# Optimization experiments

Hardware: AMD Instinct MI355X
Metric: run time of the kernel (lower is better)

## Reference

```python
import jax, jax.numpy as jnp
import numpy as np

B, NS, NQ = 128, 128, 512
D_IN, D_OUT = 256, 64


def setup_inputs() -> dict:
    key = jax.random.key(0)
    ks = jax.random.split(key, 6)
    return {
        "phi_support": jax.random.normal(ks[0], (B, NS, D_IN), dtype=jnp.float32),
        "y_support": jax.random.normal(ks[1], (B, NS, D_OUT), dtype=jnp.float32),
        "phi_query": jax.random.normal(ks[2], (B, NQ, D_IN), dtype=jnp.float32),
        "y_query": jax.random.normal(ks[3], (B, NQ, D_OUT), dtype=jnp.float32),
        # xavier-uniform-ish params
        "m_prior": jax.random.uniform(ks[4], (D_IN, D_OUT), minval=-1.0, maxval=1.0) * np.sqrt(6.0 / (D_IN + D_OUT)),
        "S_inv_prior_asym": jax.random.uniform(ks[5], (D_IN, D_IN), minval=-1.0, maxval=1.0) * np.sqrt(6.0 / (2 * D_IN)),
        "sig_eps": jnp.array([0.1], dtype=jnp.float32),
    }


def reference(phi_support, y_support, phi_query, y_query, m_prior, S_inv_prior_asym, sig_eps):
    alpha = 1.0
    d_out = m_prior.shape[1]
    # prior precision (symmetric PSD by construction) and natural-param prior mean
    S_inv_prior = alpha * (S_inv_prior_asym @ S_inv_prior_asym.T)          # [D_in, D_in]
    m_prior_nat = S_inv_prior @ m_prior                                     # [D_in, D_out]
    # posterior precision / covariance per task (nobs > 0 branch)
    S_inv = jnp.einsum('bni,bnj->bij', phi_support, phi_support) + S_inv_prior  # [B, D_in, D_in]
    S = jnp.linalg.inv(S_inv)                                               # batched small inverse
    rhs = jnp.einsum('bni,bnk->bik', phi_support, y_support) + m_prior_nat  # [B, D_in, D_out]
    m = S @ rhs                                                             # [B, D_in, D_out]
    # predictive mean and spread
    mu = phi_query @ m                                                      # [B, Q, D_out]
    spread_fac = 1.0 + jnp.einsum('bqi,bij,bqj->bq', phi_query, S, phi_query)  # [B, Q]
    # sig = spread_fac (x) (eye * sig_eps) : diagonal [B, Q, D_out, D_out]
    diag = jnp.eye(d_out, dtype=mu.dtype) * sig_eps                         # [D_out, D_out]
    sig = spread_fac[..., None, None] * diag
    # nll: logdet of diagonal sig + quadratic form with its inverse (diag -> reciprocal)
    logdet = d_out * (jnp.log(spread_fac) + jnp.log(sig_eps))               # [B, Q]
    resid = y_query - mu
    quadf = jnp.sum(resid * resid, axis=-1) / (spread_fac * sig_eps)        # [B, Q]
    nll = logdet.mean() + quadf.mean()
    return mu, sig, nll
```

## Files before the change

### kernel.cpp

```cpp
#include <hip/hip_runtime.h>
#include <math.h>

#define B_T   128
#define NS    128
#define NQ    512
#define DIN   256
#define DOUT  64

#define MU_SIZE  (B_T*NQ*DOUT)
#define SIG_SIZE (B_T*NQ*DOUT*DOUT)
#define NLL_IDX  (MU_SIZE + SIG_SIZE)

typedef double v4df __attribute__((ext_vector_type(4)));

__device__ __forceinline__ void dmap(int fl, int kq, int mrow, int rr,
                                     int& lr, int& lc) {
    if (fl == 0)      { lr = kq * 4 + rr; lc = mrow; }
    else if (fl == 1) { lr = kq + 4 * rr; lc = mrow; }
    else if (fl == 2) { lr = mrow; lc = kq * 4 + rr; }
    else              { lr = mrow; lc = kq + 4 * rr; }
}

__global__ void k_mfma_probe(double* __restrict__ FLAGD) {
    int l = threadIdx.x;
// ... 139 lines not shown
            for (int s = 0; s < 4; ++s) {
                int j = j0 + 4 * tx + s;
                Gb[i * 256 + j] = acc[r][s] + Sp[i * 256 + j];
            }
        }
    }
}

__global__ __launch_bounds__(256) void k_build_rhs(const float* __restrict__ PHI,
                                                   const float* __restrict__ Y,
                                                   const double* __restrict__ MPN,
                                                   double* __restrict__ RHS,
                                                   const double* __restrict__ FLAGD) {
    __shared__ float As[128][64];
    __shared__ float Ys[128][64];
    int b = blockIdx.x, i0 = blockIdx.y * 64, tid = threadIdx.x;
    const float* Pb = PHI + b * (NS * DIN);
    const float* Yb = Y + b * (NS * DOUT);
    for (int idx = tid; idx < 128 * 64; idx += 256) {
        int n = idx >> 6, c = idx & 63;
        As[n][c] = Pb[n * 256 + i0 + c];
        Ys[n][c] = Yb[n * 64 + c];
    }
    __syncthreads();
    double* Rb = RHS + b * 16384;
    int fl = (int)FLAGD[0];
    if (fl < 4) {
        int lane = tid & 63, w = tid >> 6;
        int mrow = lane & 15, kq = lane >> 4;
        v4df acc[4];
#pragma unroll
        for (int t = 0; t < 4; ++t) acc[t] = (v4df){0.0, 0.0, 0.0, 0.0};
        for (int ks = 0; ks < 128; ks += 4) {
            double a = (double)As[ks + kq][w * 16 + mrow];
#pragma unroll
            for (int t = 0; t < 4; ++t) {
                double bb = (double)Ys[ks + kq][t * 16 + mrow];
                acc[t] = __builtin_amdgcn_mfma_f64_16x16x4f64(a, bb, acc[t], 0, 0, 0);
            }
        }
#pragma unroll
        for (int t = 0; t < 4; ++t) {
#pragma unroll
            for (int rr = 0; rr < 4; ++rr) {
                int lr, lc; dmap(fl, kq, mrow, rr, lr, lc);
                int i = i0 + w * 16 + lr;
                int kc = t * 16 + lc;
                Rb[i * 64 + kc] = acc[t][rr] + MPN[i * 64 + kc];
            }
        }
    } else {
        int tx = tid & 15, ty = tid >> 4;
        double acc[4][4];
#pragma unroll
        for (int r = 0; r < 4; ++r)
#pragma unroll
            for (int s = 0; s < 4; ++s) acc[r][s] = 0.0;
        for (int n = 0; n < 128; ++n) {
            float a0 = As[n][4 * ty + 0], a1 = As[n][4 * ty + 1];
            float a2 = As[n][4 * ty + 2], a3 = As[n][4 * ty + 3];
            float y0 = Ys[n][4 * tx + 0], y1 = Ys[n][4 * tx + 1];
            float y2 = Ys[n][4 * tx + 2], y3 = Ys[n][4 * tx + 3];
            acc[0][0] += (double)a0 * y0; acc[0][1] += (double)a0 * y1;
            acc[0][2] += (double)a0 * y2; acc[0][3] += (double)a0 * y3;
            acc[1][0] += (double)a1 * y0; acc[1][1] += (double)a1 * y1;
            acc[1][2] += (double)a1 * y2; acc[1][3] += (double)a1 * y3;
            acc[2][0] += (double)a2 * y0; acc[2][1] += (double)a2 * y1;
            acc[2][2] += (double)a2 * y2; acc[2][3] += (double)a2 * y3;
            acc[3][0] += (double)a3 * y0; acc[3][1] += (double)a3 * y1;
            acc[3][2] += (double)a3 * y2; acc[3][3] += (double)a3 * y3;
        }
#pragma unroll
        for (int r = 0; r < 4; ++r) {
            int i = i0 + 4 * ty + r;
#pragma unroll
            for (int s = 0; s < 4; ++s) {
                int kc = 4 * tx + s;
                Rb[i * 64 + kc] = acc[r][s] + MPN[i * 64 + kc];
            }
        }
    }
}

__global__ __launch_bounds__(256) void k_potrf64(const double* __restrict__ G,
                                                 double* __restrict__ LT,
                                                 double* __restrict__ LI,
                                                 int kb) {
    __shared__ double D[64][65];
    __shared__ double T[64][33];
    __shared__ double C[32][33];
    __shared__ double L11s[16 * 17];
    __shared__ double DINVs[16];
    int b = blockIdx.x, tid = threadIdx.x;
    int o = kb * 64;
    const double* Gb = G + b * 65536;
    double* LTb = LT + b * 65536;
    double* LIb = LI + b * 16384 + kb * 4096;
    for (int idx = tid; idx < 4096; idx += 256) {
        int r = idx >> 6, c = idx & 63;
        D[r][c] = Gb[(o + r) * 256 + o + c];
    }
    __syncthreads();
    for (int p0 = 0; p0 < 64; p0 += 16) {
        if (tid < 64) {
            int lane = tid;
            double a[16];
            if (lane < 16) {
#pragma unroll
                for (int p = 0; p < 16; ++p) a[p] = D[p0 + lane][p0 + p];
            }
#pragma unroll
            for (int p = 0; p < 16; ++p) {
                double dp = __shfl(a[p], p);
                double d = sqrt(fmax(dp, 1e-300));
                double inv = 1.0 / d;
                if (lane == p) { a[p] = d; DINVs[p] = inv; }
                else if (lane > p) a[p] *= inv;
#pragma unroll
                for (int p2 = p + 1; p2 < 16; ++p2) {
                    double cc = __shfl(a[p], p2);
                    if (lane > p) a[p2] -= a[p] * cc;
                }
            }
            if (lane < 16) {
#pragma unroll
                for (int p = 0; p < 16; ++p) {
                    if (p <= lane) {
                        L11s[lane * 17 + p] = a[p];
                        D[p0 + lane][p0 + p] = a[p];
                    }
                }
            }
        }
        __syncthreads();
        int nsolve = 48 - p0;
        if (tid < nsolve) {
            int rr = p0 + 16 + tid;
            double x[16];
#pragma unroll
            for (int p = 0; p < 16; ++p) {
                double s = D[rr][p0 + p];
#pragma unroll
                for (int p2 = 0; p2 < 16; ++p2) {
                    if (p2 < p) s -= L11s[p * 17 + p2] * x[p2];
                }
                x[p] = s * DINVs[p];
                D[rr][p0 + p] = x[p];
            }
        }
        __syncthreads();
        int rem = nsolve;
        for (int idx = tid; idx < rem * rem; idx += 256) {
            int i2 = idx / rem, j2 = idx - i2 * rem;
            if (j2 <= i2) {
                int i = p0 + 16 + i2, j = p0 + 16 + j2;
                double s = 0.0;
#pragma unroll
                for (int p = 0; p < 16; ++p) s += D[i][p0 + p] * D[j][p0 + p];
                D[i][j] -= s;
            }
        }
        __syncthreads();
    }
    for (int idx = tid; idx < 4096; idx += 256) {
        int c = idx >> 6, r = idx & 63;
        if (r >= c) LTb[(o + c) * 256 + (o + r)] = D[r][c];
    }
    if (tid < 64) {
        int g = tid >> 5, j = tid & 31;
        int off = g * 32;
        double x[32];
#pragma unroll
        for (int i = 0; i < 32; ++i) {
            double s = (i == j) ? 1.0 : 0.0;
#pragma unroll
            for (int k = 0; k < i; ++k) {
                double lv = D[off + i][off + k];
                s -= (k >= j) ? lv * x[k] : 0.0;
            }
            double inv = 1.0 / D[off + i][off + i];
            x[i] = (i >= j) ? s * inv : 0.0;
        }
#pragma unroll
        for (int i = 0; i < 32; ++i) T[off + i][j] = x[i];
    }
    __syncthreads();
    for (int idx = tid; idx < 1024; idx += 256) {
        int r = idx >> 5, c = idx & 31;
        double s = 0.0;
#pragma unroll
        for (int p = 0; p < 32; ++p) s += D[32 + r][p] * T[p][c];
        C[r][c] = s;
    }
    __syncthreads();
    for (int idx = tid; idx < 1024; idx += 256) {
        int r = idx >> 5, c = idx & 31;
        double s = 0.0;
#pragma unroll
        for (int p = 0; p < 32; ++p) s += T[32 + r][p] * C[p][c];
        D[32 + r][c] = -s;
    }
    __syncthreads();
    for (int idx = tid; idx < 4096; idx += 256) {
        int p = idx >> 6, c = idx & 63;
        double v;
        if (c < 32) v = (p < 32) ? T[c][p] : 0.0;
        else        v = (p < 32) ? D[c][p] : T[c][p - 32];
        LIb[p * 64 + c] = v;
    }
}

__global__ __launch_bounds__(256) void k_trsm64(const double* __restrict__ G,
                                                const double* __restrict__ LI,
                                                double* __restrict__ LT,
                                                int kb,
                                                const double* __restrict__ FLAGD) {
    __shared__ double Gs[64][65];
    __shared__ double Ls[64][65];
    int b = blockIdx.x;
    int i0 = (kb + 1 + blockIdx.y) * 64;
    int o = kb * 64;
    int tid = threadIdx.x;
    const double* Gb = G + b * 65536;
    const double* LIb = LI + b * 16384 + kb * 4096;
    double* LTb = LT + b * 65536;
    for (int idx = tid; idx < 4096; idx += 256) {
        int r = idx >> 6, c = idx & 63;
        Gs[r][c] = Gb[(i0 + r) * 256 + o + c];
        Ls[r][c] = LIb[idx];
    }
    __syncthreads();
    int fl = (int)FLAGD[0];
    if (fl < 4) {
        int lane = tid & 63, w = tid >> 6;
        int mrow = lane & 15, kq = lane >> 4;
        v4df acc[4];
#pragma unroll
        for (int t = 0; t < 4; ++t) acc[t] = (v4df){0.0, 0.0, 0.0, 0.0};
        for (int ks = 0; ks < 64; ks += 4) {
            double a = Gs[w * 16 + mrow][ks + kq];
#pragma unroll
            for (int t = 0; t < 4; ++t) {
                double bb = Ls[ks + kq][t * 16 + mrow];
                acc[t] = __builtin_amdgcn_mfma_f64_16x16x4f64(a, bb, acc[t], 0, 0, 0);
            }
        }
#pragma unroll
        for (int t = 0; t < 4; ++t) {
#pragma unroll
            for (int rr = 0; rr < 4; ++rr) {
                int lr, lc; dmap(fl, kq, mrow, rr, lr, lc);
                int r = w * 16 + lr;
                int c = t * 16 + lc;
                LTb[(o + c) * 256 + i0 + r] = acc[t][rr];
            }
        }
    } else {
        int tx = tid & 15, ty = tid >> 4;
        double acc[4][4];
#pragma unroll
        for (int r = 0; r < 4; ++r)
#pragma unroll
            for (int s = 0; s < 4; ++s) acc[r][s] = 0.0;
        for (int kk = 0; kk < 64; ++kk) {
            double a0 = Gs[4 * ty + 0][kk], a1 = Gs[4 * ty + 1][kk];
            double a2 = Gs[4 * ty + 2][kk], a3 = Gs[4 * ty + 3][kk];
            double b0 = Ls[kk][4 * tx + 0], b1 = Ls[kk][4 * tx + 1];
            double b2 = Ls[kk][4 * tx + 2], b3 = Ls[kk][4 * tx + 3];
            acc[0][0] += a0 * b0; acc[0][1] += a0 * b1; acc[0][2] += a0 * b2; acc[0][3] += a0 * b3;
            acc[1][0] += a1 * b0; acc[1][1] += a1 * b1; acc[1][2] += a1 * b2; acc[1][3] += a1 * b3;
            acc[2][0] += a2 * b0; acc[2][1] += a2 * b1; acc[2][2] += a2 * b2; acc[2][3] += a2 * b3;
            acc[3][0] += a3 * b0; acc[3][1] += a3 * b1; acc[3][2] += a3 * b2; acc[3][3] += a3 * b3;
        }
#pragma unroll
        for (int r = 0; r < 4; ++r)
#pragma unroll
            for (int s = 0; s < 4; ++s)
                LTb[(o + 4 * tx + s) * 256 + i0 + 4 * ty + r] = acc[r][s];
    }
}

__global__ __launch_bounds__(256) void k_syrk64(const double* __restrict__ LT,
                                                double* __restrict__ G,
                                                int kb,
                                                const double* __restrict__ FLAGD) {
    __shared__ double LiT[64][65];
    __shared__ double LjT[64][65];
    int b = blockIdx.x, py = blockIdx.y;
    int ti = 0;
    while (((ti + 1) * (ti + 2)) / 2 <= py) ti++;
    int tj = py - (ti * (ti + 1)) / 2;
    int i0 = (kb + 1 + ti) * 64, j0 = (kb + 1 + tj) * 64;
    int o = kb * 64;
    int tid = threadIdx.x;
    const double* LTb = LT + b * 65536;
    double* Gb = G + b * 65536;
    for (int idx = tid; idx < 4096; idx += 256) {
        int p = idx >> 6, r = idx & 63;
        LiT[p][r] = LTb[(o + p) * 256 + i0 + r];
        LjT[p][r] = LTb[(o + p) * 256 + j0 + r];
    }
    __syncthreads();
    int fl = (int)FLAGD[0];
    if (fl < 4) {
        int lane = tid & 63, w = tid >> 6;
        int mrow = lane & 15, kq = lane >> 4;
        v4df acc[4];
#pragma unroll
        for (int t = 0; t < 4; ++t) acc[t] = (v4df){0.0, 0.0, 0.0, 0.0};
        for (int ks = 0; ks < 64; ks += 4) {
            double a = LiT[ks + kq][w * 16 + mrow];
#pragma unroll
            for (int t = 0; t < 4; ++t) {
                double bb = LjT[ks + kq][t * 16 + mrow];
                acc[t] = __builtin_amdgcn_mfma_f64_16x16x4f64(a, bb, acc[t], 0, 0, 0);
            }
        }
#pragma unroll
        for (int t = 0; t < 4; ++t) {
#pragma unroll
            for (int rr = 0; rr < 4; ++rr) {
                int lr, lc; dmap(fl, kq, mrow, rr, lr, lc);
                int gi = i0 + w * 16 + lr;
                int gj = j0 + t * 16 + lc;
                Gb[gi * 256 + gj] -= acc[t][rr];
            }
        }
    } else {
        int tx = tid & 15, ty = tid >> 4;
        double acc[4][4];
#pragma unroll
        for (int r = 0; r < 4; ++r)
#pragma unroll
            for (int s = 0; s < 4; ++s) acc[r][s] = 0.0;
        for (int kk = 0; kk < 64; ++kk) {
            double a0 = LiT[kk][4 * ty + 0], a1 = LiT[kk][4 * ty + 1];
            double a2 = LiT[kk][4 * ty + 2], a3 = LiT[kk][4 * ty + 3];
            double b0 = LjT[kk][4 * tx + 0], b1 = LjT[kk][4 * tx + 1];
            double b2 = LjT[kk][4 * tx + 2], b3 = LjT[kk][4 * tx + 3];
            acc[0][0] += a0 * b0; acc[0][1] += a0 * b1; acc[0][2] += a0 * b2; acc[0][3] += a0 * b3;
            acc[1][0] += a1 * b0; acc[1][1] += a1 * b1; acc[1][2] += a1 * b2; acc[1][3] += a1 * b3;
            acc[2][0] += a2 * b0; acc[2][1] += a2 * b1; acc[2][2] += a2 * b2; acc[2][3] += a2 * b3;
            acc[3][0] += a3 * b0; acc[3][1] += a3 * b1; acc[3][2] += a3 * b2; acc[3][3] += a3 * b3;
        }
#pragma unroll
        for (int r = 0; r < 4; ++r) {
            int gi = i0 + 4 * ty + r;
#pragma unroll
            for (int s = 0; s < 4; ++s) {
                int gj = j0 + 4 * tx + s;
                Gb[gi * 256 + gj] -= acc[r][s];
            }
        }
    }
}

__global__ __launch_bounds__(256) void k_diaginv(const double* __restrict__ LT,
                                                 double* __restrict__ TI,
                                                 float* __restrict__ TIF) {
    __shared__ double SHD[8192];
    int b = blockIdx.x, tid = threadIdx.x;
    const double* LTb = LT + b * 65536;
    double* TIb = TI + b * 65536;
    float* TIFb = TIF + b * 65536;
    for (int idx = tid; idx < 65536; idx += 256) {
        int i = idx >> 8, k = idx & 255;
        if (k > i) { TIb[idx] = 0.0; TIFb[idx] = 0.0f; }
    }
    for (int idx = tid; idx < 8192; idx += 256) {
        int g = idx >> 10, rem = idx & 1023, k = rem >> 5, i = rem & 31;
        SHD[idx] = LTb[(32 * g + k) * 256 + 32 * g + i];
    }
    __syncthreads();
    int g = tid >> 5, j = tid & 31;
    const double* D = SHD + g * 1024;
    double x[32];
#pragma unroll
    for (int i = 0; i < 32; ++i) {
        double s = (i == j) ? 1.0 : 0.0;
#pragma unroll
        for (int k = 0; k < i; ++k) {
            double lv = D[k * 32 + i];
            s -= (k >= j) ? lv * x[k] : 0.0;
        }
        double inv = 1.0 / D[i * 32 + i];
        x[i] = (i >= j) ? s * inv : 0.0;
    }
#pragma unroll
    for (int i = 0; i < 32; ++i) {
        int gi = 32 * g + i, gj = 32 * g + j;
        TIb[gi * 256 + gj] = x[i];
        TIFb[gi * 256 + gj] = (float)x[i];
    }
}

__global__ __launch_bounds__(256) void k_trinv(const double* __restrict__ LT,
                                               double* __restrict__ TI,
                                               float* __restrict__ TIF) {
    __shared__ double XS[8][1024];
    int b = blockIdx.x, J = blockIdx.y;
    int tid = threadIdx.x, j = tid & 31, ig = tid >> 5;
    const double* LTb = LT + b * 65536;
    double* TIb = TI + b * 65536;
    float* TIFb = TIF + b * 65536;
    double* Bsh = XS[7];

    for (int idx = tid; idx < 1024; idx += 256) {
        int kk = idx >> 5, c = idx & 31;
        XS[J][idx] = TIb[(32 * J + kk) * 256 + 32 * J + c];
    }
    __syncthreads();

    for (int I = J + 1; I < 8; ++I) {
        double acc[4] = {0.0, 0.0, 0.0, 0.0};
        for (int K = J; K < I; ++K) {
            for (int idx = tid; idx < 1024; idx += 256) {
                int kk = idx >> 5, i2 = idx & 31;
                Bsh[idx] = LTb[(32 * K + kk) * 256 + 32 * I + i2];
            }
            __syncthreads();
            const double* Xk = XS[K];
            for (int kk = 0; kk < 32; ++kk) {
                double tv = Xk[kk * 32 + j];
#pragma unroll
                for (int r = 0; r < 4; ++r)
                    acc[r] += Bsh[kk * 32 + ig * 4 + r] * tv;
            }
            __syncthreads();
        }
#pragma unroll
        for (int r = 0; r < 4; ++r) Bsh[(ig * 4 + r) * 32 + j] = acc[r];
        __syncthreads();
        double c[4] = {0.0, 0.0, 0.0, 0.0};
        for (int k = 0; k < 32; ++k) {
            double bv = Bsh[k * 32 + j];
#pragma unroll
            for (int r = 0; r < 4; ++r)
                c[r] -= TIb[(32 * I + ig * 4 + r) * 256 + 32 * I + k] * bv;
        }
#pragma unroll
        for (int r = 0; r < 4; ++r) {
            int gi = 32 * I + ig * 4 + r, gj = 32 * J + j;
            TIb[gi * 256 + gj] = c[r];
            TIFb[gi * 256 + gj] = (float)c[r];
            if (I < 7) XS[I][(ig * 4 + r) * 32 + j] = c[r];
        }
        __syncthreads();
    }
}

__global__ __launch_bounds__(256) void k_gemm_Z(const double* __restrict__ TI,
                                                const double* __restrict__ RHS,
                                                double* __restrict__ Z,
                                                const double* __restrict__ FLAGD) {
    __shared__ double As[64][65];
    __shared__ double Bs[64][65];
    int b = blockIdx.x, i0 = blockIdx.y * 64;
    int tid = threadIdx.x;
    const double* TIb = TI + b * 65536;
    const double* Rb = RHS + b * 16384;
    double* Zb = Z + b * 16384;
    int fl = (int)FLAGD[0];
    if (fl < 4) {
        int lane = tid & 63, w = tid >> 6;
        int mrow = lane & 15, kq = lane >> 4;
        v4df acc[4];
#pragma unroll
        for (int t = 0; t < 4; ++t) acc[t] = (v4df){0.0, 0.0, 0.0, 0.0};
        for (int k0 = 0; k0 <= i0; k0 += 64) {
            for (int idx = tid; idx < 4096; idx += 256) {
                int r = idx >> 6, kk = idx & 63;
                As[r][kk] = TIb[(i0 + r) * 256 + k0 + kk];
                Bs[r][kk] = Rb[(k0 + r) * 64 + kk];
            }
            __syncthreads();
            for (int ks = 0; ks < 64; ks += 4) {
                double a = As[w * 16 + mrow][ks + kq];
#pragma unroll
                for (int t = 0; t < 4; ++t) {
                    double bb = Bs[ks + kq][t * 16 + mrow];
                    acc[t] = __builtin_amdgcn_mfma_f64_16x16x4f64(a, bb, acc[t], 0, 0, 0);
                }
            }
            __syncthreads();
        }
#pragma unroll
        for (int t = 0; t < 4; ++t) {
#pragma unroll
            for (int rr = 0; rr < 4; ++rr) {
                int lr, lc; dmap(fl, kq, mrow, rr, lr, lc);
                Zb[(i0 + w * 16 + lr) * 64 + t * 16 + lc] = acc[t][rr];
            }
        }
    } else {
        int c = tid & 63, rg = tid >> 6;
        double acc[16];
#pragma unroll
        for (int r = 0; r < 16; ++r) acc[r] = 0.0;
        for (int k0 = 0; k0 <= i0; k0 += 64) {
            for (int idx = tid; idx < 4096; idx += 256) {
                int r = idx >> 6, kk = idx & 63;
                As[r][kk] = TIb[(i0 + r) * 256 + k0 + kk];
                Bs[r][kk] = Rb[(k0 + r) * 64 + kk];
            }
            __syncthreads();
            for (int kk = 0; kk < 64; ++kk) {
                double bv = Bs[kk][c];
#pragma unroll
                for (int r = 0; r < 16; ++r)
                    acc[r] += As[rg * 16 + r][kk] * bv;
            }
            __syncthreads();
        }
#pragma unroll
        for (int r = 0; r < 16; ++r)
            Zb[(i0 + rg * 16 + r) * 64 + c] = acc[r];
    }
}

__global__ __launch_bounds__(256) void k_gemm_M(const double* __restrict__ TI,
                                                const double* __restrict__ Z,
                                                double* __restrict__ M,
                                                const double* __restrict__ FLAGD) {
    __shared__ double As[64][65];
    __shared__ double Bs[64][65];
    int b = blockIdx.x, i0 = blockIdx.y * 64;
    int tid = threadIdx.x;
    const double* TIb = TI + b * 65536;
// ... 151 lines not shown
        float dx = y.x - v.x, dy = y.y - v.y, dz = y.z - v.z, dw = y.w - v.w;
        float qs = dx * dx + dy * dy + dz * dz + dw * dw;
        qs += __shfl_down(qs, 8, 16);
        qs += __shfl_down(qs, 4, 16);
        qs += __shfl_down(qs, 2, 16);
        qs += __shfl_down(qs, 1, 16);
        if (tx == 0) {
            float sp = 1.0f + PSUM[(size_t)(b * 4 + 0) * 512 + q]
                            + PSUM[(size_t)(b * 4 + 1) * 512 + q]
                            + PSUM[(size_t)(b * 4 + 2) * 512 + q]
                            + PSUM[(size_t)(b * 4 + 3) * 512 + q];
            SPREAD[b * 512 + q] = sp;
            float val = 64.0f * (logf(sp) + logf(se)) + qs / (sp * se);
            nred[ty * 4 + r] = (double)val;
        }
    }
    __syncthreads();
    for (int s = 32; s > 0; s >>= 1) {
        if (tid < s) nred[tid] += nred[tid + s];
        __syncthreads();
    }
    if (tid == 0) atomicAdd(NLLACC, nred[0] * (1.0 / 65536.0));
}

__global__ void k_nll_final(const double* __restrict__ NLLACC,
                            float* __restrict__ out) {
    if (threadIdx.x == 0) out[NLL_IDX] = (float)NLLACC[0];
}

__global__ __launch_bounds__(256) void k_sig(const float* __restrict__ SPREAD,
                                             const float* __restrict__ SE,
                                             float* __restrict__ out) {
    __shared__ float sv_s;
    int bq = blockIdx.x, tid = threadIdx.x;
    if (tid == 0) sv_s = SPREAD[bq] * SE[0];
    __syncthreads();
    float sv = sv_s;
    float* base = out + (size_t)MU_SIZE + (size_t)bq * 4096;
    int i = tid >> 2;
    int jb = (tid & 3) << 4;
    int d = i - jb;
    float vals[16];
#pragma unroll
    for (int t = 0; t < 16; ++t) vals[t] = (t == d) ? sv : 0.0f;
    float4* p = (float4*)(base + tid * 16);
    p[0] = make_float4(vals[0], vals[1], vals[2], vals[3]);
    p[1] = make_float4(vals[4], vals[5], vals[6], vals[7]);
    p[2] = make_float4(vals[8], vals[9], vals[10], vals[11]);
    p[3] = make_float4(vals[12], vals[13], vals[14], vals[15]);
}

extern "C" void kernel_launch(void* const* d_in, const int* in_sizes, int n_in,
                              void* d_out, int out_size, void* d_ws, size_t ws_size,
                              hipStream_t stream) {
    const float* PHI_S = (const float*)d_in[0];
    const float* Y_S   = (const float*)d_in[1];
    const float* PHI_Q = (const float*)d_in[2];
    const float* Y_Q   = (const float*)d_in[3];
    const float* MP    = (const float*)d_in[4];
    const float* AP    = (const float*)d_in[5];
    const float* SE    = (const float*)d_in[6];
    float* out = (float*)d_out;

    double* scratch = (double*)(out + MU_SIZE);
    double* G    = scratch;
    double* LT   = G + 8388608;
    double* RHS  = LT + 8388608;
    double* Z    = RHS + 2097152;
    double* TI   = Z + 2097152;
    double* Spd  = TI + 8388608;
    double* MPN  = Spd + 65536;
    double* LI   = MPN + 16384;
    float*  TIF  = (float*)(LI + 2097152);
    float*  PSUM = TIF + 8388608;
    float*  SPREAD = (float*)d_ws;
    double* NLLACC = (double*)((char*)d_ws + 65536 * 4);
    double* FLAGD  = (double*)((char*)d_ws + 65536 * 4 + 8);

    k_mfma_probe <<<1, 64, 0, stream>>>(FLAGD);
    k_prior_sp   <<<256, 256, 0, stream>>>(AP, Spd, NLLACC);
    k_prior_mpn  <<<256, 64, 0, stream>>>(Spd, MP, MPN);
    k_build_G    <<<dim3(B_T, 10), 256, 0, stream>>>(PHI_S, Spd, G, FLAGD);
    k_build_rhs  <<<dim3(B_T, 4), 256, 0, stream>>>(PHI_S, Y_S, MPN, RHS, FLAGD);
    const int syrk_pairs[3] = {6, 3, 1};
    for (int kb = 0; kb < 4; ++kb) {
        k_potrf64<<<B_T, 256, 0, stream>>>(G, LT, LI, kb);
        if (kb < 3) {
            k_trsm64<<<dim3(B_T, 3 - kb), 256, 0, stream>>>(G, LI, LT, kb, FLAGD);
            k_syrk64<<<dim3(B_T, syrk_pairs[kb]), 256, 0, stream>>>(LT, G, kb, FLAGD);
        }
    }
    k_diaginv    <<<B_T, 256, 0, stream>>>(LT, TI, TIF);
    k_trinv      <<<dim3(B_T, 7), 256, 0, stream>>>(LT, TI, TIF);
    k_gemm_Z     <<<dim3(B_T, 4), 256, 0, stream>>>(TI, RHS, Z, FLAGD);
    k_gemm_M     <<<dim3(B_T, 4), 256, 0, stream>>>(TI, Z, RHS, FLAGD);
    k_spread_gemm<<<dim3(B_T, 8, 4), 256, 0, stream>>>(PHI_Q, TIF, PSUM);
    k_mu_nll     <<<dim3(B_T, 8), 256, 0, stream>>>(PHI_Q, RHS, Y_Q, PSUM, SE,
                                                    SPREAD, NLLACC, out);
    k_nll_final  <<<1, 64, 0, stream>>>(NLLACC, out);
    k_sig        <<<65536, 256, 0, stream>>>(SPREAD, SE, out);
}
```

Baseline: 2.074 ms.

## Fuse blocked Cholesky into one per-batch kernel and use 64-wide triangular inverse

Replaces the per-panel potrf/trsm/syrk launch sequence (about ten launches) with a single kernel per batch. That kernel loops over the four 64-column panels and does the factor, the panel solve and the trailing update in place. The triangular inverse moves from 32-wide blocks to 64-wide blocks, reusing the per-panel diagonal inverses LI from the Cholesky step. The aim is to cut launch overhead and redundant diagonal inversion. In exchange, it serialises all work within one block per batch (only 128 blocks), drops the MFMA f64 path in favour of scalar FMA loops, and loses cross-block parallelism in trsm/syrk.

```diff
diff --git a/kernel.cpp b/kernel.cpp
--- a/kernel.cpp
+++ b/kernel.cpp
@@ -245,368 +245,321 @@
     }
 }
 
-__global__ __launch_bounds__(256) void k_potrf64(const double* __restrict__ G,
-                                                 double* __restrict__ LT,
-                                                 double* __restrict__ LI,
-                                                 int kb) {
-    __shared__ double D[64][65];
-    __shared__ double T[64][33];
-    __shared__ double C[32][33];
-    __shared__ double L11s[16 * 17];
-    __shared__ double DINVs[16];
+__global__ __launch_bounds__(256) void k_cholf(double* __restrict__ G,
+                                               double* __restrict__ LT,
+                                               double* __restrict__ LI) {
+    __shared__ double S[8192];
+#define DD(r, c)  S[(r) * 65 + (c)]
+#define TT(i, j)  S[4160 + (i) * 33 + (j)]
+#define CC(r, c)  S[6272 + (r) * 33 + (c)]
+    double* LL = S + 7328;
+    double* DV = S + 7600;
+    double* S1 = S;
+    double* S2 = S + 4096;
     int b = blockIdx.x, tid = threadIdx.x;
-    int o = kb * 64;
-    const double* Gb = G + b * 65536;
+    double* Gb = G + b * 65536;
     double* LTb = LT + b * 65536;
-    double* LIb = LI + b * 16384 + kb * 4096;
-    for (int idx = tid; idx < 4096; idx += 256) {
-        int r = idx >> 6, c = idx & 63;
-        D[r][c] = Gb[(o + r) * 256 + o + c];
-    }
-    __syncthreads();
-    for (int p0 = 0; p0 < 64; p0 += 16) {
+    double* LIbase = LI + b * 16384;
+
+    for (int kb = 0; kb < 4; ++kb) {
+        int o = kb * 64;
+        double* LIb = LIbase + kb * 4096;
+        for (int idx = tid; idx < 4096; idx += 256) {
+            int r = idx >> 6, c = idx & 63;
+            DD(r, c) = Gb[(o + r) * 256 + o + c];
+        }
+        __syncthreads();
+        for (int p0 = 0; p0 < 64; p0 += 16) {
+            if (tid < 64) {
+                int lane = tid;
+                double a[16];
+                if (lane < 16) {
+#pragma unroll
+                    for (int p = 0; p < 16; ++p) a[p] = DD(p0 + lane, p0 + p);
+                }
+#pragma unroll
+                for (int p = 0; p < 16; ++p) {
+                    double dp = __shfl(a[p], p);
+                    double d = sqrt(fmax(dp, 1e-300));
+                    double inv = 1.0 / d;
+                    if (lane == p) { a[p] = d; DV[p] = inv; }
+                    else if (lane > p) a[p] *= inv;
+#pragma unroll
+                    for (int p2 = p + 1; p2 < 16; ++p2) {
+                        double cc = __shfl(a[p], p2);
+                        if (lane > p) a[p2] -= a[p] * cc;
+                    }
+                }
+                if (lane < 16) {
+#pragma unroll
+                    for (int p = 0; p < 16; ++p) {
+                        if (p <= lane) {
+                            LL[lane * 17 + p] = a[p];
+                            DD(p0 + lane, p0 + p) = a[p];
+                        }
+                    }
+                }
+            }
+            __syncthreads();
+            int nsolve = 48 - p0;
+            if (tid < nsolve) {
+                int rr = p0 + 16 + tid;
+                double x[16];
+#pragma unroll
+                for (int p = 0; p < 16; ++p) {
+                    double s = DD(rr, p0 + p);
+#pragma unroll
+                    for (int p2 = 0; p2 < 16; ++p2) {
+                        if (p2 < p) s -= LL[p * 17 + p2] * x[p2];
+                    }
+                    x[p] = s * DV[p];
+                    DD(rr, p0 + p) = x[p];
+                }
+            }
+            __syncthreads();
+            int rem = nsolve;
+            for (int idx = tid; idx < rem * rem; idx += 256) {
+                int i2 = idx / rem, j2 = idx - i2 * rem;
+                if (j2 <= i2) {
+                    int i = p0 + 16 + i2, j = p0 + 16 + j2;
+                    double s = 0.0;
+#pragma unroll
+                    for (int p = 0; p < 16; ++p) s += DD(i, p0 + p) * DD(j, p0 + p);
+                    DD(i, j) -= s;
+                }
+            }
+            __syncthreads();
+        }
+        for (int idx = tid; idx < 4096; idx += 256) {
+            int c = idx >> 6, r = idx & 63;
+            if (r >= c) LTb[(o + c) * 256 + (o + r)] = DD(r, c);
+        }
         if (tid < 64) {
-            int lane = tid;
-            double a[16];
-            if (lane < 16) {
-#pragma unroll
-                for (int p = 0; p < 16; ++p) a[p] = D[p0 + lane][p0 + p];
-            }
-#pragma unroll
-            for (int p = 0; p < 16; ++p) {
-                double dp = __shfl(a[p], p);
-                double d = sqrt(fmax(dp, 1e-300));
-                double inv = 1.0 / d;
-                if (lane == p) { a[p] = d; DINVs[p] = inv; }
-                else if (lane > p) a[p] *= inv;
-#pragma unroll
-                for (int p2 = p + 1; p2 < 16; ++p2) {
-                    double cc = __shfl(a[p], p2);
-                    if (lane > p) a[p2] -= a[p] * cc;
-                }
-            }
-            if (lane < 16) {
-#pragma unroll
-                for (int p = 0; p < 16; ++p) {
-                    if (p <= lane) {
-                        L11s[lane * 17 + p] = a[p];
-                        D[p0 + lane][p0 + p] = a[p];
+            int g = tid >> 5, j = tid & 31;
+            int off = g * 32;
+            double x[32];
+#pragma unroll
+            for (int i = 0; i < 32; ++i) {
+                double s = (i == j) ? 1.0 : 0.0;
+#pragma unroll
+                for (int k = 0; k < i; ++k) {
+                    double lv = DD(off + i, off + k);
+                    s -= (k >= j) ? lv * x[k] : 0.0;
+                }
+                double inv = 1.0 / DD(off + i, off + i);
+                x[i] = (i >= j) ? s * inv : 0.0;
+            }
+#pragma unroll
+            for (int i = 0; i < 32; ++i) TT(off + i, j) = x[i];
+        }
+        __syncthreads();
+        for (int idx = tid; idx < 1024; idx += 256) {
+            int r = idx >> 5, c = idx & 31;
+            double s = 0.0;
+#pragma unroll
+            for (int p = 0; p < 32; ++p) s += DD(32 + r, p) * TT(p, c);
+            CC(r, c) = s;
+        }
+        __syncthreads();
+        for (int idx = tid; idx < 1024; idx += 256) {
+            int r = idx >> 5, c = idx & 31;
+            double s = 0.0;
+#pragma unroll
+            for (int p = 0; p < 32; ++p) s += TT(32 + r, p) * CC(p, c);
+            DD(32 + r, c) = -s;
+        }
+        __syncthreads();
+        double v[16];
+#pragma unroll
+        for (int u = 0; u < 16; ++u) {
+            int idx = tid + u * 256;
+            int p = idx >> 6, c = idx & 63;
+            v[u] = (c < 32) ? ((p < 32) ? TT(c, p) : 0.0)
+                            : ((p < 32) ? DD(c, p) : TT(c, p - 32));
+        }
+        __syncthreads();
+#pragma unroll
+        for (int u = 0; u < 16; ++u) S1[tid + u * 256] = v[u];
+        __syncthreads();
+        for (int idx = tid; idx < 4096; idx += 256) LIb[idx] = S1[idx];
+        for (int rb = kb + 1; rb < 4; ++rb) {
+            int i0 = rb * 64;
+            for (int idx = tid; idx < 4096; idx += 256) {
+                int r = idx >> 6, kk = idx & 63;
+                S2[kk * 64 + r] = Gb[(i0 + r) * 256 + o + kk];
+            }
+            __syncthreads();
+            int tx = tid & 15, ty = tid >> 4;
+            double acc[4][4];
+#pragma unroll
+            for (int r = 0; r < 4; ++r)
+#pragma unroll
+                for (int s = 0; s < 4; ++s) acc[r][s] = 0.0;
+            for (int kk = 0; kk < 64; ++kk) {
+                double a0 = S2[kk * 64 + 4 * ty + 0], a1 = S2[kk * 64 + 4 * ty + 1];
+                double a2 = S2[kk * 64 + 4 * ty + 2], a3 = S2[kk * 64 + 4 * ty + 3];
+                double b0 = S1[kk * 64 + 4 * tx + 0], b1 = S1[kk * 64 + 4 * tx + 1];
+                double b2 = S1[kk * 64 + 4 * tx + 2], b3 = S1[kk * 64 + 4 * tx + 3];
+                acc[0][0] += a0 * b0; acc[0][1] += a0 * b1; acc[0][2] += a0 * b2; acc[0][3] += a0 * b3;
+                acc[1][0] += a1 * b0; acc[1][1] += a1 * b1; acc[1][2] += a1 * b2; acc[1][3] += a1 * b3;
+                acc[2][0] += a2 * b0; acc[2][1] += a2 * b1; acc[2][2] += a2 * b2; acc[2][3] += a2 * b3;
+                acc[3][0] += a3 * b0; acc[3][1] += a3 * b1; acc[3][2] += a3 * b2; acc[3][3] += a3 * b3;
+            }
+#pragma unroll
+            for (int r = 0; r < 4; ++r)
+#pragma unroll
+                for (int s = 0; s < 4; ++s)
+                    LTb[(o + 4 * tx + s) * 256 + i0 + 4 * ty + r] = acc[r][s];
+            __syncthreads();
+        }
+        for (int ti2 = kb + 1; ti2 < 4; ++ti2) {
+            for (int tj2 = kb + 1; tj2 <= ti2; ++tj2) {
+                int i0 = ti2 * 64, j0 = tj2 * 64;
+                for (int idx = tid; idx < 4096; idx += 256) {
+                    int p = idx >> 6, r = idx & 63;
+                    S1[idx] = LTb[(o + p) * 256 + i0 + r];
+                    S2[idx] = LTb[(o + p) * 256 + j0 + r];
+                }
+                __syncthreads();
+                int tx = tid & 15, ty = tid >> 4;
+                double acc[4][4];
+#pragma unroll
+                for (int r = 0; r < 4; ++r)
+#pragma unroll
+                    for (int s = 0; s < 4; ++s) acc[r][s] = 0.0;
+                for (int kk = 0; kk < 64; ++kk) {
+                    double a0 = S1[kk * 64 + 4 * ty + 0], a1 = S1[kk * 64 + 4 * ty + 1];
+                    double a2 = S1[kk * 64 + 4 * ty + 2], a3 = S1[kk * 64 + 4 * ty + 3];
+                    double b0 = S2[kk * 64 + 4 * tx + 0], b1 = S2[kk * 64 + 4 * tx + 1];
+                    double b2 = S2[kk * 64 + 4 * tx + 2], b3 = S2[kk * 64 + 4 * tx + 3];
+                    acc[0][0] += a0 * b0; acc[0][1] += a0 * b1; acc[0][2] += a0 * b2; acc[0][3] += a0 * b3;
+                    acc[1][0] += a1 * b0; acc[1][1] += a1 * b1; acc[1][2] += a1 * b2; acc[1][3] += a1 * b3;
+                    acc[2][0] += a2 * b0; acc[2][1] += a2 * b1; acc[2][2] += a2 * b2; acc[2][3] += a2 * b3;
+                    acc[3][0] += a3 * b0; acc[3][1] += a3 * b1; acc[3][2] += a3 * b2; acc[3][3] += a3 * b3;
+                }
+#pragma unroll
+                for (int r = 0; r < 4; ++r) {
+                    int gi = i0 + 4 * ty + r;
+#pragma unroll
+                    for (int s = 0; s < 4; ++s) {
+                        int gj = j0 + 4 * tx + s;
+                        Gb[gi * 256 + gj] -= acc[r][s];
                     }
                 }
-            }
-        }
-        __syncthreads();
-        int nsolve = 48 - p0;
-        if (tid < nsolve) {
-            int rr = p0 + 16 + tid;
-            double x[16];
-#pragma unroll
-            for (int p = 0; p < 16; ++p) {
-                double s = D[rr][p0 + p];
-#pragma unroll
-                for (int p2 = 0; p2 < 16; ++p2) {
-                    if (p2 < p) s -= L11s[p * 17 + p2] * x[p2];
-                }
-                x[p] = s * DINVs[p];
-                D[rr][p0 + p] = x[p];
-            }
-        }
-        __syncthreads();
-        int rem = nsolve;
-        for (int idx = tid; idx < rem * rem; idx += 256) {
-            int i2 = idx / rem, j2 = idx - i2 * rem;
-            if (j2 <= i2) {
-                int i = p0 + 16 + i2, j = p0 + 16 + j2;
-                double s = 0.0;
-#pragma unroll
-                for (int p = 0; p < 16; ++p) s += D[i][p0 + p] * D[j][p0 + p];
-                D[i][j] -= s;
-            }
-        }
-        __syncthreads();
-    }
-    for (int idx = tid; idx < 4096; idx += 256) {
-        int c = idx >> 6, r = idx & 63;
-        if (r >= c) LTb[(o + c) * 256 + (o + r)] = D[r][c];
-    }
-    if (tid < 64) {
-        int g = tid >> 5, j = tid & 31;
-        int off = g * 32;
-        double x[32];
-#pragma unroll
-        for (int i = 0; i < 32; ++i) {
-            double s = (i == j) ? 1.0 : 0.0;
-#pragma unroll
-            for (int k = 0; k < i; ++k) {
-                double lv = D[off + i][off + k];
-                s -= (k >= j) ? lv * x[k] : 0.0;
-            }
-            double inv = 1.0 / D[off + i][off + i];
-            x[i] = (i >= j) ? s * inv : 0.0;
-        }
-#pragma unroll
-        for (int i = 0; i < 32; ++i) T[off + i][j] = x[i];
-    }
-    __syncthreads();
-    for (int idx = tid; idx < 1024; idx += 256) {
-        int r = idx >> 5, c = idx & 31;
-        double s = 0.0;
-#pragma unroll
-        for (int p = 0; p < 32; ++p) s += D[32 + r][p] * T[p][c];
-        C[r][c] = s;
-    }
-    __syncthreads();
-    for (int idx = tid; idx < 1024; idx += 256) {
-        int r = idx >> 5, c = idx & 31;
-        double s = 0.0;
-#pragma unroll
-        for (int p = 0; p < 32; ++p) s += T[32 + r][p] * C[p][c];
-        D[32 + r][c] = -s;
-    }
-    __syncthreads();
-    for (int idx = tid; idx < 4096; idx += 256) {
-        int p = idx >> 6, c = idx & 63;
-        double v;
-        if (c < 32) v = (p < 32) ? T[c][p] : 0.0;
-        else        v = (p < 32) ? D[c][p] : T[c][p - 32];
-        LIb[p * 64 + c] = v;
-    }
-}
-
-__global__ __launch_bounds__(256) void k_trsm64(const double* __restrict__ G,
-                                                const double* __restrict__ LI,
-                                                double* __restrict__ LT,
-                                                int kb,
-                                                const double* __restrict__ FLAGD) {
-    __shared__ double Gs[64][65];
-    __shared__ double Ls[64][65];
-    int b = blockIdx.x;
-    int i0 = (kb + 1 + blockIdx.y) * 64;
-    int o = kb * 64;
-    int tid = threadIdx.x;
-    const double* Gb = G + b * 65536;
-    const double* LIb = LI + b * 16384 + kb * 4096;
-    double* LTb = LT + b * 65536;
-    for (int idx = tid; idx < 4096; idx += 256) {
-        int r = idx >> 6, c = idx & 63;
-        Gs[r][c] = Gb[(i0 + r) * 256 + o + c];
-        Ls[r][c] = LIb[idx];
-    }
-    __syncthreads();
-    int fl = (int)FLAGD[0];
-    if (fl < 4) {
-        int lane = tid & 63, w = tid >> 6;
-        int mrow = lane & 15, kq = lane >> 4;
-        v4df acc[4];
-#pragma unroll
-        for (int t = 0; t < 4; ++t) acc[t] = (v4df){0.0, 0.0, 0.0, 0.0};
-        for (int ks = 0; ks < 64; ks += 4) {
-            double a = Gs[w * 16 + mrow][ks + kq];
-#pragma unroll
-            for (int t = 0; t < 4; ++t) {
-                double bb = Ls[ks + kq][t * 16 + mrow];
-                acc[t] = __builtin_amdgcn_mfma_f64_16x16x4f64(a, bb, acc[t], 0, 0, 0);
-            }
-        }
-#pragma unroll
-        for (int t = 0; t < 4; ++t) {
-#pragma unroll
-            for (int rr = 0; rr < 4; ++rr) {
-                int lr, lc; dmap(fl, kq, mrow, rr, lr, lc);
-                int r = w * 16 + lr;
-                int c = t * 16 + lc;
-                LTb[(o + c) * 256 + i0 + r] = acc[t][rr];
-            }
-        }
-    } else {
-        int tx = tid & 15, ty = tid >> 4;
-        double acc[4][4];
-#pragma unroll
-        for (int r = 0; r < 4; ++r)
-#pragma unroll
-            for (int s = 0; s < 4; ++s) acc[r][s] = 0.0;
-        for (int kk = 0; kk < 64; ++kk) {
-            double a0 = Gs[4 * ty + 0][kk], a1 = Gs[4 * ty + 1][kk];
-            double a2 = Gs[4 * ty + 2][kk], a3 = Gs[4 * ty + 3][kk];
-            double b0 = Ls[kk][4 * tx + 0], b1 = Ls[kk][4 * tx + 1];
-            double b2 = Ls[kk][4 * tx + 2], b3 = Ls[kk][4 * tx + 3];
-            acc[0][0] += a0 * b0; acc[0][1] += a0 * b1; acc[0][2] += a0 * b2; acc[0][3] += a0 * b3;
-            acc[1][0] += a1 * b0; acc[1][1] += a1 * b1; acc[1][2] += a1 * b2; acc[1][3] += a1 * b3;
-            acc[2][0] += a2 * b0; acc[2][1] += a2 * b1; acc[2][2] += a2 * b2; acc[2][3] += a2 * b3;
-            acc[3][0] += a3 * b0; acc[3][1] += a3 * b1; acc[3][2] += a3 * b2; acc[3][3] += a3 * b3;
-        }
-#pragma unroll
-        for (int r = 0; r < 4; ++r)
-#pragma unroll
-            for (int s = 0; s < 4; ++s)
-                LTb[(o + 4 * tx + s) * 256 + i0 + 4 * ty + r] = acc[r][s];
-    }
-}
-
-__global__ __launch_bounds__(256) void k_syrk64(const double* __restrict__ LT,
-                                                double* __restrict__ G,
-                                                int kb,
-                                                const double* __restrict__ FLAGD) {
-    __shared__ double LiT[64][65];
-    __shared__ double LjT[64][65];
-    int b = blockIdx.x, py = blockIdx.y;
-    int ti = 0;
-    while (((ti + 1) * (ti + 2)) / 2 <= py) ti++;
-    int tj = py - (ti * (ti + 1)) / 2;
-    int i0 = (kb + 1 + ti) * 64, j0 = (kb + 1 + tj) * 64;
-    int o = kb * 64;
-    int tid = threadIdx.x;
-    const double* LTb = LT + b * 65536;
-    double* Gb = G + b * 65536;
-    for (int idx = tid; idx < 4096; idx += 256) {
-        int p = idx >> 6, r = idx & 63;
-        LiT[p][r] = LTb[(o + p) * 256 + i0 + r];
-        LjT[p][r] = LTb[(o + p) * 256 + j0 + r];
-    }
-    __syncthreads();
-    int fl = (int)FLAGD[0];
-    if (fl < 4) {
-        int lane = tid & 63, w = tid >> 6;
-        int mrow = lane & 15, kq = lane >> 4;
-        v4df acc[4];
-#pragma unroll
-        for (int t = 0; t < 4; ++t) acc[t] = (v4df){0.0, 0.0, 0.0, 0.0};
-        for (int ks = 0; ks < 64; ks += 4) {
-            double a = LiT[ks + kq][w * 16 + mrow];
-#pragma unroll
-            for (int t = 0; t < 4; ++t) {
-                double bb = LjT[ks + kq][t * 16 + mrow];
-                acc[t] = __builtin_amdgcn_mfma_f64_16x16x4f64(a, bb, acc[t], 0, 0, 0);
-            }
-        }
-#pragma unroll
-        for (int t = 0; t < 4; ++t) {
-#pragma unroll
-            for (int rr = 0; rr < 4; ++rr) {
-                int lr, lc; dmap(fl, kq, mrow, rr, lr, lc);
-                int gi = i0 + w * 16 + lr;
-                int gj = j0 + t * 16 + lc;
-                Gb[gi * 256 + gj] -= acc[t][rr];
-            }
-        }
-    } else {
-        int tx = tid & 15, ty = tid >> 4;
-        double acc[4][4];
-#pragma unroll
-        for (int r = 0; r < 4; ++r)
-#pragma unroll
-            for (int s = 0; s < 4; ++s) acc[r][s] = 0.0;
-        for (int kk = 0; kk < 64; ++kk) {
-            double a0 = LiT[kk][4 * ty + 0], a1 = LiT[kk][4 * ty + 1];
-            double a2 = LiT[kk][4 * ty + 2], a3 = LiT[kk][4 * ty + 3];
-            double b0 = LjT[kk][4 * tx + 0], b1 = LjT[kk][4 * tx + 1];
-            double b2 = LjT[kk][4 * tx + 2], b3 = LjT[kk][4 * tx + 3];
-            acc[0][0] += a0 * b0; acc[0][1] += a0 * b1; acc[0][2] += a0 * b2; acc[0][3] += a0 * b3;
-            acc[1][0] += a1 * b0; acc[1][1] += a1 * b1; acc[1][2] += a1 * b2; acc[1][3] += a1 * b3;
-            acc[2][0] += a2 * b0; acc[2][1] += a2 * b1; acc[2][2] += a2 * b2; acc[2][3] += a2 * b3;
-            acc[3][0] += a3 * b0; acc[3][1] += a3 * b1; acc[3][2] += a3 * b2; acc[3][3] += a3 * b3;
-        }
-#pragma unroll
-        for (int r = 0; r < 4; ++r) {
-            int gi = i0 + 4 * ty + r;
-#pragma unroll
-            for (int s = 0; s < 4; ++s) {
-                int gj = j0 + 4 * tx + s;
-                Gb[gi * 256 + gj] -= acc[r][s];
-            }
-        }
-    }
-}
-
-__global__ __launch_bounds__(256) void k_diaginv(const double* __restrict__ LT,
+                __syncthreads();
+            }
+        }
+    }
+#undef DD
+#undef TT
+#undef CC
+}
+
+__global__ __launch_bounds__(256) void k_tidiag(const double* __restrict__ LI,
+                                                double* __restrict__ TI,
+                                                float* __restrict__ TIF) {
+    __shared__ double Ls[4096];
+    int b = blockIdx.x, tid = threadIdx.x;
+    const double* LIbase = LI + b * 16384;
+    double* TIb = TI + b * 65536;
+    float* TIFb = TIF + b * 65536;
+    const int tis[6] = {0, 0, 0, 1, 1, 2};
+    const int tjs[6] = {1, 2, 3, 2, 3, 3};
+    for (int t = 0; t < 6; ++t) {
+        int o_i = tis[t] * 64, o_j = tjs[t] * 64;
+        for (int idx = tid; idx < 4096; idx += 256) {
+            int r = idx >> 6, c = idx & 63;
+            TIb[(o_i + r) * 256 + o_j + c] = 0.0;
+            TIFb[(o_i + r) * 256 + o_j + c] = 0.0f;
+        }
+    }
+    for (int kb = 0; kb < 4; ++kb) {
+        for (int idx = tid; idx < 4096; idx += 256) Ls[idx] = LIbase[kb * 4096 + idx];
+        __syncthreads();
+        int o = kb * 64;
+        for (int idx = tid; idx < 4096; idx += 256) {
+            int r = idx >> 6, c = idx & 63;
+            double vv = (c <= r) ? Ls[c * 64 + r] : 0.0;
+            TIb[(o + r) * 256 + o + c] = vv;
+            TIFb[(o + r) * 256 + o + c] = (float)vv;
+        }
+        __syncthreads();
+    }
+}
+
+__global__ __launch_bounds__(256) void k_trinv64(const double* __restrict__ LT,
+                                                 const double* __restrict__ LI,
                                                  double* __restrict__ TI,
                                                  float* __restrict__ TIF) {
-    __shared__ double SHD[8192];
-    int b = blockIdx.x, tid = threadIdx.x;
+    __shared__ double A1[4096];
+    __shared__ double A2[4096];
+    int b = blockIdx.x, J = blockIdx.y;
+    int tid = threadIdx.x, tx = tid & 15, ty = tid >> 4;
     const double* LTb = LT + b * 65536;
+    const double* LIbase = LI + b * 16384;
     double* TIb = TI + b * 65536;
     float* TIFb = TIF + b * 65536;
-    for (int idx = tid; idx < 65536; idx += 256) {
-        int i = idx >> 8, k = idx & 255;
-        if (k > i) { TIb[idx] = 0.0; TIFb[idx] = 0.0f; }
-    }
-    for (int idx = tid; idx < 8192; idx += 256) {
-        int g = idx >> 10, rem = idx & 1023, k = rem >> 5, i = rem & 31;
-        SHD[idx] = LTb[(32 * g + k) * 256 + 32 * g + i];
-    }
-    __syncthreads();
-    int g = tid >> 5, j = tid & 31;
-    const double* D = SHD + g * 1024;
-    double x[32];
-#pragma unroll
-    for (int i = 0; i < 32; ++i) {
-        double s = (i == j) ? 1.0 : 0.0;
-#pragma unroll
-        for (int k = 0; k < i; ++k) {
-            double lv = D[k * 32 + i];
-            s -= (k >= j) ? lv * x[k] : 0.0;
-        }
-        double inv = 1.0 / D[i * 32 + i];
-        x[i] = (i >= j) ? s * inv : 0.0;
-    }
-#pragma unroll
-    for (int i = 0; i < 32; ++i) {
-        int gi = 32 * g + i, gj = 32 * g + j;
-        TIb[gi * 256 + gj] = x[i];
-        TIFb[gi * 256 + gj] = (float)x[i];
-    }
-}
-
-__global__ __launch_bounds__(256) void k_trinv(const double* __restrict__ LT,
-                                               double* __restrict__ TI,
-                                               float* __restrict__ TIF) {
-    __shared__ double XS[8][1024];
-    int b = blockIdx.x, J = blockIdx.y;
-    int tid = threadIdx.x, j = tid & 31, ig = tid >> 5;
-    const double* LTb = LT + b * 65536;
-    double* TIb = TI + b * 65536;
-    float* TIFb = TIF + b * 65536;
-    double* Bsh = XS[7];
-
-    for (int idx = tid; idx < 1024; idx += 256) {
-        int kk = idx >> 5, c = idx & 31;
-        XS[J][idx] = TIb[(32 * J + kk) * 256 + 32 * J + c];
-    }
-    __syncthreads();
-
-    for (int I = J + 1; I < 8; ++I) {
-        double acc[4] = {0.0, 0.0, 0.0, 0.0};
+    int oJ = J * 64;
+    for (int I = J + 1; I < 4; ++I) {
+        int oI = I * 64;
+        double acc[4][4];
+#pragma unroll
+        for (int r = 0; r < 4; ++r)
+#pragma unroll
+            for (int s = 0; s < 4; ++s) acc[r][s] = 0.0;
         for (int K = J; K < I; ++K) {
-            for (int idx = tid; idx < 1024; idx += 256) {
-                int kk = idx >> 5, i2 = idx & 31;
-                Bsh[idx] = LTb[(32 * K + kk) * 256 + 32 * I + i2];
-            }
-            __syncthreads();
-            const double* Xk = XS[K];
-            for (int kk = 0; kk < 32; ++kk) {
-                double tv = Xk[kk * 32 + j];
-#pragma unroll
-                for (int r = 0; r < 4; ++r)
-                    acc[r] += Bsh[kk * 32 + ig * 4 + r] * tv;
-            }
-            __syncthreads();
-        }
-#pragma unroll
-        for (int r = 0; r < 4; ++r) Bsh[(ig * 4 + r) * 32 + j] = acc[r];
-        __syncthreads();
-        double c[4] = {0.0, 0.0, 0.0, 0.0};
-        for (int k = 0; k < 32; ++k) {
-            double bv = Bsh[k * 32 + j];
-#pragma unroll
-            for (int r = 0; r < 4; ++r)
-                c[r] -= TIb[(32 * I + ig * 4 + r) * 256 + 32 * I + k] * bv;
+            int oK = K * 64;
+            for (int idx = tid; idx < 4096; idx += 256) {
+                int k = idx >> 6, x = idx & 63;
+                A1[idx] = LTb[(oK + k) * 256 + oI + x];
+                A2[idx] = TIb[(oK + k) * 256 + oJ + x];
+            }
+            __syncthreads();
+            for (int kk = 0; kk < 64; ++kk) {
+                double a0 = A1[kk * 64 + 4 * ty + 0], a1 = A1[kk * 64 + 4 * ty + 1];
+                double a2 = A1[kk * 64 + 4 * ty + 2], a3 = A1[kk * 64 + 4 * ty + 3];
+                double b0 = A2[kk * 64 + 4 * tx + 0], b1 = A2[kk * 64 + 4 * tx + 1];
+                double b2 = A2[kk * 64 + 4 * tx + 2], b3 = A2[kk * 64 + 4 * tx + 3];
+                acc[0][0] += a0 * b0; acc[0][1] += a0 * b1; acc[0][2] += a0 * b2; acc[0][3] += a0 * b3;
+                acc[1][0] += a1 * b0; acc[1][1] += a1 * b1; acc[1][2] += a1 * b2; acc[1][3] += a1 * b3;
+                acc[2][0] += a2 * b0; acc[2][1] += a2 * b1; acc[2][2] += a2 * b2; acc[2][3] += a2 * b3;
+                acc[3][0] += a3 * b0; acc[3][1] += a3 * b1; acc[3][2] += a3 * b2; acc[3][3] += a3 * b3;
+            }
+            __syncthreads();
+        }
+#pragma unroll
+        for (int r = 0; r < 4; ++r)
+#pragma unroll
+            for (int s = 0; s < 4; ++s)
+                A2[(4 * ty + r) * 64 + 4 * tx + s] = acc[r][s];
+        for (int idx = tid; idx < 4096; idx += 256)
+            A1[idx] = LIbase[I * 4096 + idx];
+        __syncthreads();
+        double c2[4][4];
+#pragma unroll
+        for (int r = 0; r < 4; ++r)
+#pragma unroll
+            for (int s = 0; s < 4; ++s) c2[r][s] = 0.0;
+        for (int kk = 0; kk < 64; ++kk) {
+            double a0 = A1[kk * 64 + 4 * ty + 0], a1 = A1[kk * 64 + 4 * ty + 1];
+            double a2 = A1[kk * 64 + 4 * ty + 2], a3 = A1[kk * 64 + 4 * ty + 3];
+            double b0 = A2[kk * 64 + 4 * tx + 0], b1 = A2[kk * 64 + 4 * tx + 1];
+            double b2 = A2[kk * 64 + 4 * tx + 2], b3 = A2[kk * 64 + 4 * tx + 3];
+            c2[0][0] += a0 * b0; c2[0][1] += a0 * b1; c2[0][2] += a0 * b2; c2[0][3] += a0 * b3;
+            c2[1][0] += a1 * b0; c2[1][1] += a1 * b1; c2[1][2] += a1 * b2; c2[1][3] += a1 * b3;
+            c2[2][0] += a2 * b0; c2[2][1] += a2 * b1; c2[2][2] += a2 * b2; c2[2][3] += a2 * b3;
+            c2[3][0] += a3 * b0; c2[3][1] += a3 * b1; c2[3][2] += a3 * b2; c2[3][3] += a3 * b3;
         }
 #pragma unroll
         for (int r = 0; r < 4; ++r) {
-            int gi = 32 * I + ig * 4 + r, gj = 32 * J + j;
-            TIb[gi * 256 + gj] = c[r];
-            TIFb[gi * 256 + gj] = (float)c[r];
-            if (I < 7) XS[I][(ig * 4 + r) * 32 + j] = c[r];
+            int gi = oI + 4 * ty + r;
+#pragma unroll
+            for (int s = 0; s < 4; ++s) {
+                int gj = oJ + 4 * tx + s;
+                double xv = -c2[r][s];
+                TIb[gi * 256 + gj] = xv;
+                TIFb[gi * 256 + gj] = (float)xv;
+            }
         }
         __syncthreads();
     }
@@ -924,16 +877,9 @@
     k_prior_mpn  <<<256, 64, 0, stream>>>(Spd, MP, MPN);
     k_build_G    <<<dim3(B_T, 10), 256, 0, stream>>>(PHI_S, Spd, G, FLAGD);
     k_build_rhs  <<<dim3(B_T, 4), 256, 0, stream>>>(PHI_S, Y_S, MPN, RHS, FLAGD);
-    const int syrk_pairs[3] = {6, 3, 1};
-    for (int kb = 0; kb < 4; ++kb) {
-        k_potrf64<<<B_T, 256, 0, stream>>>(G, LT, LI, kb);
-        if (kb < 3) {
-            k_trsm64<<<dim3(B_T, 3 - kb), 256, 0, stream>>>(G, LI, LT, kb, FLAGD);
-            k_syrk64<<<dim3(B_T, syrk_pairs[kb]), 256, 0, stream>>>(LT, G, kb, FLAGD);
-        }
-    }
-    k_diaginv    <<<B_T, 256, 0, stream>>>(LT, TI, TIF);
-    k_trinv      <<<dim3(B_T, 7), 256, 0, stream>>>(LT, TI, TIF);
+    k_cholf      <<<B_T, 256, 0, stream>>>(G, LT, LI);
+    k_tidiag     <<<B_T, 256, 0, stream>>>(LI, TI, TIF);
+    k_trinv64    <<<dim3(B_T, 3), 256, 0, stream>>>(LT, LI, TI, TIF);
     k_gemm_Z     <<<dim3(B_T, 4), 256, 0, stream>>>(TI, RHS, Z, FLAGD);
     k_gemm_M     <<<dim3(B_T, 4), 256, 0, stream>>>(TI, Z, RHS, FLAGD);
     k_spread_gemm<<<dim3(B_T, 8, 4), 256, 0, stream>>>(PHI_Q, TIF, PSUM);
```

After: 2.259 ms. +8.9%, slower.
